# Kernel optimization log

Hardware: AMD Instinct MI355X
Metric: run time of the kernel (lower is better)

The kernel has to match this reference:

```python
import jax, jax.numpy as jnp
import numpy as np

B, P, K, KS = 512, 64, 30, 4      # graphs, nodes per graph, sort-pool k, conv1d kernel
N, E, F, H = B * P, 524288, 128, 256
N_CLASSES = 10
L_OUT = K - KS + 1                 # 27, conv1d output length


def _sage(h, wl, wr, b, src, dst, inv_deg):
    # PyG SAGEConv (mean aggr): out = lin_l(mean_j x_j) + lin_r(x_i); bias only on lin_l
    agg = jax.ops.segment_sum(h[src], dst, num_segments=N) * inv_deg
    return jax.nn.relu(agg @ wl + b + h @ wr)


def setup_inputs() -> dict:
    key = jax.random.key(0)
    ks = jax.random.split(key, 32)
    x = jax.random.normal(ks[0], (N, F), jnp.float32)
    # intra-graph random edges (src -> dst aggregation)
    g = jax.random.randint(ks[1], (E,), 0, B)
    src = g * P + jax.random.randint(ks[2], (E,), 0, P)
    dst = g * P + jax.random.randint(ks[3], (E,), 0, P)
    edge_index = jnp.stack([src, dst]).astype(jnp.int32)
    batch = jnp.repeat(jnp.arange(B), P).astype(jnp.int32)  # sorted graph ids

    def lin(k, i, o):
        return jax.random.normal(k, (i, o), jnp.float32) / np.float32(np.sqrt(i))

    inp = {"x": x, "edge_index": edge_index, "batch": batch}
    dims = [(F, H), (H, H), (H, H), (H, H)]
    ki = 4
    for li, (i, o) in enumerate(dims):
        inp[f"sage{li}_wl"] = lin(ks[ki], i, o); ki += 1
        inp[f"sage{li}_wr"] = lin(ks[ki], i, o); ki += 1
        inp[f"sage{li}_b"] = jnp.zeros((o,), jnp.float32)
    inp["conv1d_w"] = jax.random.normal(ks[ki], (H, H, KS), jnp.float32) / np.float32(np.sqrt(H * KS)); ki += 1
    inp["conv1d_b"] = jnp.zeros((H,), jnp.float32)
    inp["lin1_w"] = lin(ks[ki], H * L_OUT, H); ki += 1
    inp["lin1_b"] = jnp.zeros((H,), jnp.float32)
    inp["lin2_w"] = lin(ks[ki], H, 128); ki += 1
    inp["lin2_b"] = jnp.zeros((128,), jnp.float32)
    inp["out_w"] = lin(ks[ki], 128, N_CLASSES); ki += 1
    inp["out_b"] = jnp.zeros((N_CLASSES,), jnp.float32)
    return inp


def reference(x, edge_index, batch,
              sage0_wl, sage0_wr, sage0_b,
              sage1_wl, sage1_wr, sage1_b,
              sage2_wl, sage2_wr, sage2_b,
              sage3_wl, sage3_wr, sage3_b,
              conv1d_w, conv1d_b, lin1_w, lin1_b,
              lin2_w, lin2_b, out_w, out_b):
    src, dst = edge_index[0], edge_index[1]
    deg = jax.ops.segment_sum(jnp.ones(src.shape, x.dtype), dst, num_segments=N)
    inv_deg = (1.0 / jnp.maximum(deg, 1.0))[:, None]

    h = jnp.nan_to_num(x, nan=0.0)
    h = _sage(h, sage0_wl, sage0_wr, sage0_b, src, dst, inv_deg)
    h = _sage(h, sage1_wl, sage1_wr, sage1_b, src, dst, inv_deg)
    h = _sage(h, sage2_wl, sage2_wr, sage2_b, src, dst, inv_deg)
    h = _sage(h, sage3_wl, sage3_wr, sage3_b, src, dst, inv_deg)  # [N, H]

    # SortAggregation(k=K): to dense batch, sort by last channel desc, top-k, zero-pad
    counts = jax.ops.segment_sum(jnp.ones(N, jnp.int32), batch, num_segments=B)
    offsets = jnp.cumsum(counts) - counts
    pos = jnp.arange(N) - offsets[batch]
    D = h.shape[1]
    dense = jnp.zeros((B, P, D), h.dtype).at[batch, pos].set(h)
    valid = jnp.zeros((B, P), bool).at[batch, pos].set(True)
    skey = jnp.where(valid, dense[..., -1], -jnp.inf)
    order = jnp.argsort(-skey, axis=1)[:, :K]                       # [B, K]
    topk = jnp.take_along_axis(dense, order[..., None], axis=1)     # [B, K, D]
    tvalid = jnp.take_along_axis(valid, order, axis=1)
    topk = jnp.where(tvalid[..., None], topk, 0.0)

    # x.view(B, K, -1).permute(0, 2, 1) -> [B, D, K]
    xc = topk.transpose(0, 2, 1)
    y = jax.lax.conv_general_dilated(xc, conv1d_w, (1,), 'VALID',
                                     dimension_numbers=('NCH', 'OIH', 'NCH'))
    y = jax.nn.relu(y + conv1d_b[None, :, None])                    # [B, H, L_OUT]
    y = y.reshape(B, -1)                                            # dropout is identity in eval
    y = jax.nn.relu(y @ lin1_w + lin1_b)
    y = jax.nn.relu(y @ lin2_w + lin2_b)
    return jax.nn.relu(y @ out_w + out_b)                           # [B, N_CLASSES]
```

## Files before the change

kernel.cpp:

```cpp
#include <hip/hip_runtime.h>
#include <hip/hip_bf16.h>

#define NNODES 32768
#define NEDGES 524288
#define NGRAPH 512
#define PNODES 64
#define KTOP 30
#define FIN 128
#define HID 256
#define LOUT 27

#define C1F 4.8828125e-4f
#define C2F 2.384185791015625e-7f

using f16x8 = __attribute__((ext_vector_type(8))) _Float16;
using f16x4 = __attribute__((ext_vector_type(4))) _Float16;
using f32x4 = __attribute__((ext_vector_type(4))) float;
using f32x16 = __attribute__((ext_vector_type(16))) float;
using u32x4 = __attribute__((ext_vector_type(4))) uint32_t;

template<int N> struct IC { static constexpr int v = N; };

#define GLDS(src, dst) __builtin_amdgcn_global_load_lds( \
    (const __attribute__((address_space(1))) void*)(src), \
    (__attribute__((address_space(3))) void*)(dst), 16, 0, 0)

__global__ void hist_kernel(const int* __restrict__ dst, int* __restrict__ counts) {
    int e = blockIdx.x * blockDim.x + threadIdx.x;
    if (e < NEDGES) atomicAdd(&counts[dst[e]], 1);
}

__global__ __launch_bounds__(1024) void scan_block_kernel(const int* __restrict__ counts,
        int* __restrict__ loc, int* __restrict__ partial) {
    int b = blockIdx.x, t = threadIdx.x;
    int i = b * 1024 + t;
    int v = counts[i];
    int lane = t & 63, w = t >> 6;
    int x = v;
    #pragma unroll
    for (int d = 1; d < 64; d <<= 1) { int y = __shfl_up(x, d, 64); if (lane >= d) x += y; }
    __shared__ int ws[16];
    if (lane == 63) ws[w] = x;
    __syncthreads();
    if (w == 0) {
        int s = (lane < 16) ? ws[lane] : 0;
        #pragma unroll
        for (int d = 1; d < 16; d <<= 1) { int y = __shfl_up(s, d, 64); if (lane >= d) s += y; }
        if (lane < 16) ws[lane] = s;
    }
    __syncthreads();
    int base = (w > 0) ? ws[w - 1] : 0;
    int incl = base + x;
    loc[i] = incl - v;
    if (t == 1023) partial[b] = incl;
}

__global__ __launch_bounds__(1024) void scan_fixup_kernel(const int* __restrict__ loc,
        const int* __restrict__ partial, const int* __restrict__ counts,
        int* __restrict__ offsets, int* __restrict__ cursor, float* __restrict__ invdeg) {
    int b = blockIdx.x, t = threadIdx.x;
    int i = b * 1024 + t;
    __shared__ int sbase;
    if (t == 0) { int s = 0; for (int j = 0; j < b; ++j) s += partial[j]; sbase = s; }
    __syncthreads();
    int o = loc[i] + sbase;
    offsets[i] = o;
    cursor[i] = o;
    invdeg[i] = 1.0f / fmaxf((float)counts[i], 1.0f);
}

__global__ void scatter_kernel(const int* __restrict__ src, const int* __restrict__ dst,
        int* __restrict__ cursor, int* __restrict__ ssrc) {
    int e = blockIdx.x * blockDim.x + threadIdx.x;
    if (e < NEDGES) {
        int d = dst[e];
        int p = atomicAdd(&cursor[d], 1);
        ssrc[p] = ((d & 63) << 6) | (src[e] & 63);
    }
}

struct PrepSage {
    const float* src[8];
    _Float16* dh[8];
    _Float16* dl[8];
    int logK[8];
    int part[8];
};

struct PrepAll {
    const float* x;
    _Float16* h0h; _Float16* h0l;
    PrepSage ps;
    const float* convw; _Float16* cvh; _Float16* cvl;
    const float* l1w; _Float16* w1h; _Float16* w1l;
};

__global__ __launch_bounds__(256) void prep_all_kernel(PrepAll P) {
    __shared__ float sh[64][65];
    const int b = blockIdx.x, t = threadIdx.x;
    if (b < 4096) {
        int i = b * 256 + t;
        float4 v = *(const float4*)(P.x + (size_t)i * 4);
        float xs[4] = {v.x, v.y, v.z, v.w};
        f16x4 hh, ll;
        #pragma unroll
        for (int q = 0; q < 4; ++q) {
            float a = xs[q];
            a = (a != a) ? 0.f : a;
            _Float16 h = (_Float16)a;
            hh[q] = h;
            ll[q] = (_Float16)((a - (float)h) * 2048.0f);
        }
        *(f16x4*)(P.h0h + (size_t)i * 4) = hh;
        *(f16x4*)(P.h0l + (size_t)i * 4) = ll;
    } else if (b < 6144) {
        int seg = b - 4096;
        int y = seg >> 8;
        int idx = (seg & 255) * 256 + t;
        int lk = P.ps.logK[y], K = 1 << lk;
        if (idx < 256 * K) {
            int n = idx >> lk, k = idx & (K - 1);
            float w = P.ps.src[y][(size_t)k * 256 + n];
            _Float16 h = (_Float16)w;
            int wv = n >> 5, l31 = n & 31;
            int c = k >> 5, h2 = (k >> 4) & 1, hb = (k >> 3) & 1, j = k & 7;
            int NCH = K >> 5;
            size_t dst = (size_t)(wv * 2 + P.ps.part[y]) * (size_t)(NCH * 1024)
                       + (size_t)(c * 2 + h2) * 512 + (size_t)(hb * 32 + l31) * 8 + j;
            P.ps.dh[y][dst] = h;
            P.ps.dl[y][dst] = (_Float16)((w - (float)h) * 2048.0f);
        }
    } else if (b < 7168) {
        int idx = (b - 6144) * 256 + t;
        int o = idx >> 10, k = idx & 1023;
        float w = P.convw[(size_t)o * 1024 + (k & 255) * 4 + (k >> 8)];
        _Float16 h = (_Float16)w;
        P.cvh[(size_t)o * 1024 + k] = h;
        P.cvl[(size_t)o * 1024 + k] = (_Float16)((w - (float)h) * 2048.0f);
    } else {
        int seg = b - 7168;
        int kb = (seg % 108) * 64;
        int nb = (seg / 108) * 64;
        {
            int kk = t >> 2;
            int nc = (t & 3) * 16;
            int k = kb + kk, l = k >> 8, c = k & 255;
            const float* srow = P.l1w + (size_t)(c * 27 + l) * 256 + nb + nc;
            #pragma unroll
            for (int j = 0; j < 16; j += 4) {
                float4 v = *(const float4*)(srow + j);
                sh[kk][nc + j + 0] = v.x;
                sh[kk][nc + j + 1] = v.y;
                sh[kk][nc + j + 2] = v.z;
                sh[kk][nc + j + 3] = v.w;
            }
        }
        __syncthreads();
        {
            int nn = t >> 2;
            int kc = (t & 3) * 16;
            f16x8 oh[2], ol[2];
            #pragma unroll
            for (int j = 0; j < 16; ++j) {
                float x = sh[kc + j][nn];
                _Float16 h = (_Float16)x;
                oh[j >> 3][j & 7] = h;
                ol[j >> 3][j & 7] = (_Float16)((x - (float)h) * 2048.0f);
            }
            size_t o = (size_t)(nb + nn) * 6912 + kb + kc;
            *(f16x8*)(P.w1h + o) = oh[0];
            *(f16x8*)(P.w1h + o + 8) = oh[1];
            *(f16x8*)(P.w1l + o) = ol[0];
            *(f16x8*)(P.w1l + o + 8) = ol[1];
        }
    }
}

struct SageWAll {
    const _Float16* wh[4];
    const _Float16* wl[4];
    const float* bias[4];
};

__global__ __launch_bounds__(512, 2) void fused_sage_all_kernel(
        const _Float16* __restrict__ hh, const _Float16* __restrict__ hl,
        const int* __restrict__ offsets, const int* __restrict__ counts,
        const int* __restrict__ ssrc, const float* __restrict__ invdeg,
        SageWAll W,
        _Float16* __restrict__ tkh, _Float16* __restrict__ tkl) {
    __shared__ __align__(16) _Float16 hp[2][8 * 2048];
    __shared__ __align__(16) uint32_t Sw[4096];
    const int g = blockIdx.x, t = threadIdx.x;
    const int lane = t & 63, wave = t >> 6;
    const int l31 = lane & 31, hb = lane >> 5;

    #pragma unroll
    for (int i = 0; i < 8; ++i) Sw[t + i * 512] = 0;

    {
        int a = lane >> 2, b = lane & 3;
        #pragma unroll
        for (int u0 = 0; u0 < 4; ++u0) {
            int u = u0 * 8 + wave;
            int part = u & 1;
            int cs = u >> 1;
            int c = cs >> 2, stripe = cs & 3;
            int row = stripe * 16 + a;
            int o = b ^ ((row >> 1) & 3) ^ (c & 3);
            const _Float16* src = (part ? hl : hh) + (size_t)g * (64 * FIN)
                                + (size_t)row * FIN + c * 32 + o * 8;
            GLDS(src, &hp[part][c * 2048 + stripe * 512]);
        }
    }
    const int gbeg = offsets[g * 64];
    const int gend = offsets[g * 64 + 63] + counts[g * 64 + 63];
    __syncthreads();

    for (int e = gbeg + t; e < gend; e += 512)
        atomicAdd(&Sw[ssrc[e] & 4095], 1u);
    __syncthreads();

    {
        int d = t >> 3, o = t & 7;
        float idg = invdeg[g * 64 + d];
        float v[8];
        #pragma unroll
        for (int j = 0; j < 8; ++j) v[j] = (float)Sw[(d << 6) + (o << 3) + j] * idg;
        __syncthreads();
        _Float16* Sp = (_Float16*)Sw;
        f16x8 s0, s1;
        #pragma unroll
        for (int j = 0; j < 8; ++j) {
            _Float16 h1 = (_Float16)v[j];
            s0[j] = h1;
            s1[j] = (_Float16)((v[j] - (float)h1) * 2048.0f);
        }
        int addr = (d << 6) + ((o ^ (d & 7)) << 3);
        *(f16x8*)&Sp[addr] = s0;
        *(f16x8*)&Sp[4096 + addr] = s1;
    }
    __syncthreads();

    const int col = (wave << 5) + l31;

    auto gemmHalf = [&](auto NC, const _Float16* __restrict__ Bh,
                        const _Float16* __restrict__ Bl, int rowOff) -> f32x16 {
        constexpr int NIT = decltype(NC)::v * 2;
        const int lo8 = lane << 3;
        f32x16 a0 = 0.f, a1 = 0.f;
        f16x8 bhN = *(const f16x8*)(Bh + lo8);
        f16x8 blN = *(const f16x8*)(Bl + lo8);
        #pragma unroll
        for (int it = 0; it < NIT; ++it) {
            const int c = it >> 1, h2 = it & 1;
            f16x8 bh = bhN, bl = blN;
            if (it + 1 < NIT) {
                bhN = *(const f16x8*)(Bh + (it + 1) * 512 + lo8);
                blN = *(const f16x8*)(Bl + (it + 1) * 512 + lo8);
            }
            const int slot = (2 * h2 + hb) ^ ((l31 >> 1) & 3) ^ (c & 3);
            const int addr = rowOff + c * 2048 + (l31 << 5) + (slot << 3);
            f16x8 ah = *(const f16x8*)&hp[0][addr];
            f16x8 al = *(const f16x8*)&hp[1][addr];
            a0 = __builtin_amdgcn_mfma_f32_32x32x16_f16(ah, bh, a0, 0, 0, 0);
            a1 = __builtin_amdgcn_mfma_f32_32x32x16_f16(al, bh, a1, 0, 0, 0);
            a1 = __builtin_amdgcn_mfma_f32_32x32x16_f16(ah, bl, a1, 0, 0, 0);
        }
        return a0 + C1F * a1;
    };

    auto packpair = [](float x, float y, uint32_t& hw, uint32_t& lw) {
        _Float16 xh = (_Float16)x, yh = (_Float16)y;
        _Float16 xl = (_Float16)((x - (float)xh) * 2048.0f);
        _Float16 yl = (_Float16)((y - (float)yh) * 2048.0f);
        hw = (uint32_t)__builtin_bit_cast(unsigned short, xh)
           | ((uint32_t)__builtin_bit_cast(unsigned short, yh) << 16);
        lw = (uint32_t)__builtin_bit_cast(unsigned short, xl)
           | ((uint32_t)__builtin_bit_cast(unsigned short, yl) << 16);
    };

    auto spass = [&](int soffBase, const f32x16& pf0, const f32x16& pf1, f32x16& qf) {
        const _Float16* Sp = (const _Float16*)Sw;
        f32x16 sA = 0.f, sB = 0.f;
        #pragma unroll
        for (int kc = 0; kc < 4; ++kc) {
            const f32x16& pfk = (kc < 2) ? pf0 : pf1;
            const int i0 = ((2 * kc) & 3) * 4, i1 = ((2 * kc + 1) & 3) * 4;
            float kv0 = hb ? pfk[i1 + 0] : pfk[i0 + 0];
            float kv1 = hb ? pfk[i1 + 1] : pfk[i0 + 1];
            float kv2 = hb ? pfk[i1 + 2] : pfk[i0 + 2];
            float kv3 = hb ? pfk[i1 + 3] : pfk[i0 + 3];
            float sv0 = hb ? pfk[i0 + 0] : pfk[i1 + 0];
            float sv1 = hb ? pfk[i0 + 1] : pfk[i1 + 1];
            float sv2 = hb ? pfk[i0 + 2] : pfk[i1 + 2];
            float sv3 = hb ? pfk[i0 + 3] : pfk[i1 + 3];
            uint32_t kh0, kl0, kh1, kl1, sh0, sl0, sh1, sl1;
            packpair(kv0, kv1, kh0, kl0);
            packpair(kv2, kv3, kh1, kl1);
            packpair(sv0, sv1, sh0, sl0);
            packpair(sv2, sv3, sh1, sl1);
            uint32_t rh0 = (uint32_t)__shfl_xor((int)sh0, 32, 64);
            uint32_t rh1 = (uint32_t)__shfl_xor((int)sh1, 32, 64);
            uint32_t rl0 = (uint32_t)__shfl_xor((int)sl0, 32, 64);
            uint32_t rl1 = (uint32_t)__shfl_xor((int)sl1, 32, 64);
            u32x4 bhu, blu;
            bhu[0] = hb ? rh0 : kh0;  bhu[1] = hb ? rh1 : kh1;
            bhu[2] = hb ? kh0 : rh0;  bhu[3] = hb ? kh1 : rh1;
            blu[0] = hb ? rl0 : kl0;  blu[1] = hb ? rl1 : kl1;
            blu[2] = hb ? kl0 : rl0;  blu[3] = hb ? kl1 : rl1;
            f16x8 bhv = __builtin_bit_cast(f16x8, bhu);
            f16x8 blv = __builtin_bit_cast(f16x8, blu);
            int soff = soffBase + (l31 << 6) + (((2 * kc + hb) ^ (l31 & 7)) << 3);
            f16x8 s0a = *(const f16x8*)&Sp[soff];
            f16x8 s1a = *(const f16x8*)&Sp[4096 + soff];
            sA = __builtin_amdgcn_mfma_f32_32x32x16_f16(s0a, bhv, sA, 0, 0, 0);
            sB = __builtin_amdgcn_mfma_f32_32x32x16_f16(s0a, blv, sB, 0, 0, 0);
            sB = __builtin_amdgcn_mfma_f32_32x32x16_f16(s1a, bhv, sB, 0, 0, 0);
        }
        qf += sA + C1F * sB;
    };

    auto run_layer = [&](auto NC, const _Float16* __restrict__ Wsh,
                         const _Float16* __restrict__ Wsl,
                         const float* __restrict__ bias,
                         f32x16& sC0, f32x16& sC1) {
        constexpr size_t wstride = (size_t)decltype(NC)::v * 1024;
        const _Float16* BqH = Wsh + (size_t)((wave << 1) + 1) * wstride;
        const _Float16* BqL = Wsl + (size_t)((wave << 1) + 1) * wstride;
        const _Float16* BpH = Wsh + (size_t)(wave << 1) * wstride;
        const _Float16* BpL = Wsl + (size_t)(wave << 1) * wstride;
        f32x16 qf0 = gemmHalf(NC, BqH, BqL, 0);
        f32x16 qf1 = gemmHalf(NC, BqH, BqL, 1024);
        f32x16 pf0 = gemmHalf(NC, BpH, BpL, 0);
        f32x16 pf1 = gemmHalf(NC, BpH, BpL, 1024);
        spass(0, pf0, pf1, qf0);
        spass(2048, pf0, pf1, qf1);
        const float bb = bias[col];
        #pragma unroll
        for (int reg = 0; reg < 16; ++reg) {
            sC0[reg] = fmaxf(qf0[reg] + bb, 0.f);
            sC1[reg] = fmaxf(qf1[reg] + bb, 0.f);
        }
    };

    auto hp_write = [&](const f32x16& sC0, const f32x16& sC1) {
        int oc = l31 >> 3, j = l31 & 7;
        #pragma unroll
        for (int mi = 0; mi < 2; ++mi)
            #pragma unroll
            for (int reg = 0; reg < 16; ++reg) {
                int row = (mi << 5) + (reg & 3) + ((reg >> 2) << 3) + (hb << 2);
                int slot = oc ^ ((row >> 1) & 3) ^ (wave & 3);
                int addr = wave * 2048 + (row << 5) + (slot << 3) + j;
                float v = mi ? sC1[reg] : sC0[reg];
                _Float16 h1 = (_Float16)v;
                hp[0][addr] = h1;
                hp[1][addr] = (_Float16)((v - (float)h1) * 2048.0f);
            }
    };

    f32x16 sC0, sC1;
    run_layer(IC<4>{}, W.wh[0], W.wl[0], W.bias[0], sC0, sC1);
    __syncthreads();
    hp_write(sC0, sC1);
    __syncthreads();
    run_layer(IC<8>{}, W.wh[1], W.wl[1], W.bias[1], sC0, sC1);
    __syncthreads();
    hp_write(sC0, sC1);
    __syncthreads();
    run_layer(IC<8>{}, W.wh[2], W.wl[2], W.bias[2], sC0, sC1);
    __syncthreads();
    hp_write(sC0, sC1);
    __syncthreads();
    run_layer(IC<8>{}, W.wh[3], W.wl[3], W.bias[3], sC0, sC1);
    __syncthreads();

    #pragma unroll
    for (int mi = 0; mi < 2; ++mi) {
        #pragma unroll
        for (int reg = 0; reg < 16; ++reg) {
            int row = (mi << 5) + (reg & 3) + ((reg >> 2) << 3) + (hb << 2);
            int cx = col ^ ((((row >> 2) & 1) << 5) | ((row & 3) << 3));
            float v = mi ? sC1[reg] : sC0[reg];
            _Float16 h1 = (_Float16)v;
            hp[0][(row << 8) + cx] = h1;
            hp[1][(row << 8) + cx] = (_Float16)((v - (float)h1) * 2048.0f);
        }
    }
    __syncthreads();

    float* vals = (float*)Sw;
    int* ords = (int*)(Sw + 64);
    if (t < 64) {
        int sx = 255 ^ ((((t >> 2) & 1) << 5) | ((t & 3) << 3));
        vals[t] = (float)hp[0][(t << 8) + sx] + C1F * (float)hp[1][(t << 8) + sx];
    }
    __syncthreads();
    if (t < 64) {
        float v = vals[t];
        int rank = 0;
        for (int j = 0; j < 64; ++j) {
            float vj = vals[j];
            rank += (vj > v) || (vj == v && j < t);
        }
        if (rank < KTOP) ords[rank] = t;
    }
    __syncthreads();
    for (int r = wave; r < KTOP; r += 8) {
        int row = ords[r];
        int cc = (lane & 31) << 3;
        int sx = cc ^ ((((row >> 2) & 1) << 5) | ((row & 3) << 3));
        size_t d = (size_t)(g * KTOP + r) * HID + cc;
        if (lane < 32) *(f16x8*)(tkh + d) = *(const f16x8*)&hp[0][(row << 8) + sx];
        else           *(f16x8*)(tkl + d) = *(const f16x8*)&hp[1][(row << 8) + sx];
    }
}

template<int NPROD, int CONV, int NPAIRS, int EPI>
__global__ __launch_bounds__(256, 2) void mfma_ps_kernel(
        const _Float16* __restrict__ A1h, const _Float16* __restrict__ A1l,
        const _Float16* __restrict__ A2h, const _Float16* __restrict__ A2l,
        const _Float16* __restrict__ B1h, const _Float16* __restrict__ B1l,
        const _Float16* __restrict__ B2h, const _Float16* __restrict__ B2l,
        const float* __restrict__ bias,
        _Float16* __restrict__ outh, _Float16* __restrict__ outl,
        float* __restrict__ Cpart,
        int lda, int K, int Nd, int nrb) {
    __shared__ _Float16 As[2][2][128 * 32];
    __shared__ _Float16 Bs[2][2][128 * 32];
    const int t = threadIdx.x;
    const int lane = t & 63, wave = t >> 6;
    const int wr = wave & 1, wc = wave >> 1;
    const int bid = blockIdx.x;
    const int rb = bid % nrb, cb = bid / nrb;
    const int row0 = rb * 128, col0 = cb * 128;
    const int l31 = lane & 31, hb = lane >> 5, x3 = l31 & 3;
    const int r16 = lane >> 2;
    const int qsrc8 = ((lane & 3) ^ (r16 & 3)) * 8;
    size_t aoffj[2], boffj[2];
    #pragma unroll
    for (int j = 0; j < 2; ++j) {
        int ar = row0 + wave * 32 + j * 16 + r16;
        aoffj[j] = CONV ? ((size_t)ar * 256 + (size_t)(ar / 27) * 768)
                        : (size_t)ar * (size_t)lda;
        boffj[j] = (size_t)(col0 + wave * 32 + j * 16 + r16) * (size_t)K;
    }
    int aroff[2], broff[2], slot8[2];
    #pragma unroll
    for (int mi = 0; mi < 2; ++mi) aroff[mi] = (wr * 64 + mi * 32 + l31) * 32;
    #pragma unroll
    for (int ni = 0; ni < 2; ++ni) broff[ni] = (wc * 64 + ni * 32 + l31) * 32;
    #pragma unroll
    for (int h = 0; h < 2; ++h) slot8[h] = ((2 * h + hb) ^ x3) * 8;

    const int KV = NPAIRS * K;
    const int kchunk = KV / gridDim.z;
    const int kv_lo = blockIdx.z * kchunk, kv_hi = kv_lo + kchunk;

    f32x16 acc0[2][2], acc1[2][2], acc2[2][2];
    #pragma unroll
    for (int i = 0; i < 2; ++i)
        #pragma unroll
        for (int j = 0; j < 2; ++j) { acc0[i][j] = 0.f; acc1[i][j] = 0.f; acc2[i][j] = 0.f; }

    auto stage = [&](int kv, int b) {
        int p = (NPAIRS == 2 && kv >= K) ? 1 : 0;
        int k = kv - p * K;
        const _Float16* __restrict__ sAh = p ? A2h : A1h;
        const _Float16* __restrict__ sAl = p ? A2l : A1l;
        const _Float16* __restrict__ sBh = p ? B2h : B1h;
        const _Float16* __restrict__ sBl = p ? B2l : B1l;
        #pragma unroll
        for (int j = 0; j < 2; ++j) {
            int ldsbase = (wave * 32 + j * 16) * 32;
            size_t ga = aoffj[j] + k + qsrc8;
            size_t gb = boffj[j] + k + qsrc8;
            GLDS(sAh + ga, &As[b][0][ldsbase]);
            GLDS(sAl + ga, &As[b][1][ldsbase]);
            GLDS(sBh + gb, &Bs[b][0][ldsbase]);
            GLDS(sBl + gb, &Bs[b][1][ldsbase]);
        }
    };

    stage(kv_lo, 0);
    __syncthreads();
    int b = 0;
    for (int kv = kv_lo; kv < kv_hi; kv += 32) {
        if (kv + 32 < kv_hi) stage(kv + 32, b ^ 1);
        #pragma unroll
        for (int h = 0; h < 2; ++h) {
            f16x8 af0[2], af1[2], bf0[2], bf1[2];
            #pragma unroll
            for (int mi = 0; mi < 2; ++mi) {
                af0[mi] = *(const f16x8*)&As[b][0][aroff[mi] + slot8[h]];
                af1[mi] = *(const f16x8*)&As[b][1][aroff[mi] + slot8[h]];
            }
            #pragma unroll
            for (int ni = 0; ni < 2; ++ni) {
                bf0[ni] = *(const f16x8*)&Bs[b][0][broff[ni] + slot8[h]];
                bf1[ni] = *(const f16x8*)&Bs[b][1][broff[ni] + slot8[h]];
            }
            #pragma unroll
            for (int mi = 0; mi < 2; ++mi)
                #pragma unroll
                for (int ni = 0; ni < 2; ++ni) {
                    acc0[mi][ni] = __builtin_amdgcn_mfma_f32_32x32x16_f16(af0[mi], bf0[ni], acc0[mi][ni], 0, 0, 0);
                    acc1[mi][ni] = __builtin_amdgcn_mfma_f32_32x32x16_f16(af1[mi], bf0[ni], acc1[mi][ni], 0, 0, 0);
                    acc1[mi][ni] = __builtin_amdgcn_mfma_f32_32x32x16_f16(af0[mi], bf1[ni], acc1[mi][ni], 0, 0, 0);
                    if (NPROD == 4)
                        acc2[mi][ni] = __builtin_amdgcn_mfma_f32_32x32x16_f16(af1[mi], bf1[ni], acc2[mi][ni], 0, 0, 0);
                }
        }
        b ^= 1;
        __syncthreads();
    }

    const int rquad = 4 * hb;
    #pragma unroll
    for (int ni = 0; ni < 2; ++ni) {
        int col = col0 + wc * 64 + ni * 32 + l31;
        float bb = (EPI == 0) ? bias[col] : 0.f;
        #pragma unroll
        for (int mi = 0; mi < 2; ++mi) {
            #pragma unroll
            for (int reg = 0; reg < 16; ++reg) {
                float v = acc0[mi][ni][reg] + C1F * acc1[mi][ni][reg];
                if (NPROD == 4) v += C2F * acc2[mi][ni][reg];
                int row = row0 + wr * 64 + mi * 32 + (reg & 3) + 8 * (reg >> 2) + rquad;
                if (EPI == 0) {
                    v = fmaxf(v + bb, 0.f);
                    _Float16 h = (_Float16)v;
                    size_t o = (size_t)row * Nd + col;
                    outh[o] = h;
                    outl[o] = (_Float16)((v - (float)h) * 2048.0f);
                } else {
                    size_t zb = (size_t)blockIdx.z * (size_t)(nrb * 128) * Nd;
                    Cpart[zb + (size_t)row * Nd + col] = v;
                }
            }
        }
    }
}

__global__ void reduce_conv_kernel(const float* __restrict__ yb32,
        const float* __restrict__ b, _Float16* __restrict__ ybh, _Float16* __restrict__ ybl) {
    int i = blockIdx.x * 256 + threadIdx.x;
    float v = fmaxf(yb32[i] + yb32[i + 13824 * 256] + b[i & 255], 0.f);
    _Float16 h = (_Float16)v;
    ybh[i] = h;
    ybl[i] = (_Float16)((v - (float)h) * 2048.0f);
}

__global__ void reduce_lin1_kernel(const float* __restrict__ z1p,
        const float* __restrict__ b, float* __restrict__ z1) {
    int i = blockIdx.x * 256 + threadIdx.x;
    float s = b[i & 255];
    #pragma unroll
    for (int z = 0; z < 27; ++z) s += z1p[(size_t)z * 131072 + i];
    z1[i] = fmaxf(s, 0.f);
}

__global__ __launch_bounds__(256) void gemm64_kernel(
        const float* __restrict__ A, const float* __restrict__ B,
        const float* __restrict__ bias, float* __restrict__ C,
        int lda, int kend, int Nd) {
    __shared__ float As[16][64];
    __shared__ float Bs[16][64];
    const int tid = threadIdx.x;
    const int tx = tid & 15, ty = tid >> 4;
    const int la_r = tid >> 2, la_c = (tid & 3) << 2;
    const int lb_r = tid >> 4, lb_c = (tid & 15) << 2;
    const int row0 = blockIdx.x * 64, col0 = blockIdx.y * 64;
    const size_t aoff = (size_t)(row0 + la_r) * (size_t)lda;
    float acc[4][4] = {};
    for (int k0 = 0; k0 < kend; k0 += 16) {
        __syncthreads();
        float4 av = *(const float4*)(A + aoff + k0 + la_c);
        As[la_c + 0][la_r] = av.x;
        As[la_c + 1][la_r] = av.y;
        As[la_c + 2][la_r] = av.z;
        As[la_c + 3][la_r] = av.w;
        *(float4*)&Bs[lb_r][lb_c] = *(const float4*)(B + (size_t)(k0 + lb_r) * Nd + col0 + lb_c);
        __syncthreads();
        #pragma unroll
        for (int k = 0; k < 16; ++k) {
            float4 a = *(const float4*)&As[k][ty << 2];
            float4 b = *(const float4*)&Bs[k][tx << 2];
            acc[0][0] += a.x * b.x; acc[0][1] += a.x * b.y; acc[0][2] += a.x * b.z; acc[0][3] += a.x * b.w;
            acc[1][0] += a.y * b.x; acc[1][1] += a.y * b.y; acc[1][2] += a.y * b.z; acc[1][3] += a.y * b.w;
            acc[2][0] += a.z * b.x; acc[2][1] += a.z * b.y; acc[2][2] += a.z * b.z; acc[2][3] += a.z * b.w;
            acc[3][0] += a.w * b.x; acc[3][1] += a.w * b.y; acc[3][2] += a.w * b.z; acc[3][3] += a.w * b.w;
        }
    }
    #pragma unroll
    for (int i = 0; i < 4; ++i) {
        int row = row0 + (ty << 2) + i;
        #pragma unroll
        for (int j = 0; j < 4; ++j) {
            int col = col0 + (tx << 2) + j;
            C[(size_t)row * Nd + col] = fmaxf(acc[i][j] + bias[col], 0.f);
        }
    }
}

__global__ void out_kernel(const float* __restrict__ z2, const float* __restrict__ w,
        const float* __restrict__ b, float* __restrict__ out) {
    int idx = blockIdx.x * blockDim.x + threadIdx.x;
    if (idx < NGRAPH * 10) {
        int r = idx / 10, c = idx % 10;
        float s = b[c];
        for (int k = 0; k < 128; ++k) s += z2[r * 128 + k] * w[k * 10 + c];
        out[idx] = fmaxf(s, 0.f);
    }
}

extern "C" void kernel_launch(void* const* d_in, const int* in_sizes, int n_in,
                              void* d_out, int out_size, void* d_ws, size_t ws_size,
                              hipStream_t stream) {
    const float* x    = (const float*)d_in[0];
    const int*   edge = (const int*)d_in[1];
    const int*   esrc = edge;
    const int*   edst = edge + NEDGES;
    const float* wl[4] = {(const float*)d_in[3], (const float*)d_in[6], (const float*)d_in[9],  (const float*)d_in[12]};
    const float* wr[4] = {(const float*)d_in[4], (const float*)d_in[7], (const float*)d_in[10], (const float*)d_in[13]};
    const float* sb[4] = {(const float*)d_in[5], (const float*)d_in[8], (const float*)d_in[11], (const float*)d_in[14]};
    const float* convw = (const float*)d_in[15];
    const float* convb = (const float*)d_in[16];
    const float* l1w   = (const float*)d_in[17];
    const float* l1b   = (const float*)d_in[18];
    const float* l2w   = (const float*)d_in[19];
    const float* l2b   = (const float*)d_in[20];
    const float* ow    = (const float*)d_in[21];
    const float* ob    = (const float*)d_in[22];
    float* out = (float*)d_out;

    char* ws = (char*)d_ws;
    size_t off = 0;
    auto alloc = [&](size_t bytes) -> char* {
        char* p = ws + off;
        off = (off + bytes + 255) & ~(size_t)255;
        return p;
    };
    int*   counts  = (int*)alloc((size_t)NNODES * 4);
    int*   offsets = (int*)alloc((size_t)NNODES * 4);
    int*   cursor  = (int*)alloc((size_t)NNODES * 4);
    int*   loc     = (int*)alloc((size_t)NNODES * 4);
    int*   partial = (int*)alloc(32 * 4);
    float* invdeg  = (float*)alloc((size_t)NNODES * 4);
    int*   ssrc    = (int*)alloc((size_t)NEDGES * 4);
    _Float16* wch[4]; _Float16* wcl[4];
    for (int l = 0; l < 4; ++l) {
        size_t kb = (size_t)512 * (l ? HID : FIN) * 2;
        wch[l] = (_Float16*)alloc(kb);
        wcl[l] = (_Float16*)alloc(kb);
    }
    _Float16* cvh = (_Float16*)alloc((size_t)HID * 1024 * 2);
    _Float16* cvl = (_Float16*)alloc((size_t)HID * 1024 * 2);

    const size_t H0T = (size_t)NNODES * FIN * 2;
    const size_t AGT = (size_t)NNODES * HID * 2;
    const size_t TKT = (size_t)NGRAPH * KTOP * HID * 2;
    const size_t YBT = (size_t)NGRAPH * LOUT * HID * 2;
    const size_t YB32T = (size_t)2 * 13824 * 256 * 4;
    const size_t W1T = (size_t)HID * 6912 * 2;

    char* R1 = alloc(2 * H0T);
    char* R2 = alloc(2 * AGT);
    char* R3 = alloc(2 * AGT);
    char* R4 = alloc(2 * AGT);
    _Float16* h0h = (_Float16*)R1; _Float16* h0l = (_Float16*)(R1 + H0T);
    _Float16* tkh = (_Float16*)R4; _Float16* tkl = (_Float16*)(R4 + TKT);
    _Float16* ybh = (_Float16*)R2; _Float16* ybl_ = (_Float16*)(R2 + YBT);
    float* yb32 = (float*)(R2 + 2 * YBT);
    float* z1p  = (float*)(R2 + 2 * YBT);
    char* tail2 = R2 + 2 * YBT + YB32T;
    float* z1  = (float*)tail2;
    float* z2  = (float*)(tail2 + (size_t)NGRAPH * HID * 4);
    _Float16* w1h = (_Float16*)(tail2 + (size_t)NGRAPH * HID * 4 + (size_t)NGRAPH * 128 * 4 + 256);
    _Float16* w1l = (_Float16*)((char*)w1h + W1T);

    hipMemsetAsync(counts, 0, (size_t)NNODES * 4, stream);
    hist_kernel<<<NEDGES / 256, 256, 0, stream>>>(edst, counts);
    scan_block_kernel<<<NNODES / 1024, 1024, 0, stream>>>(counts, loc, partial);
    scan_fixup_kernel<<<NNODES / 1024, 1024, 0, stream>>>(loc, partial, counts, offsets, cursor, invdeg);
    scatter_kernel<<<NEDGES / 256, 256, 0, stream>>>(esrc, edst, cursor, ssrc);

    PrepAll pa;
    pa.x = x; pa.h0h = h0h; pa.h0l = h0l;
    for (int l = 0; l < 4; ++l) {
        int lk = l ? 8 : 7;
        pa.ps.src[2 * l] = wl[l];     pa.ps.dh[2 * l] = wch[l];     pa.ps.dl[2 * l] = wcl[l];
        pa.ps.src[2 * l + 1] = wr[l]; pa.ps.dh[2 * l + 1] = wch[l]; pa.ps.dl[2 * l + 1] = wcl[l];
        pa.ps.logK[2 * l] = lk;     pa.ps.part[2 * l] = 0;
        pa.ps.logK[2 * l + 1] = lk; pa.ps.part[2 * l + 1] = 1;
    }
    pa.convw = convw; pa.cvh = cvh; pa.cvl = cvl;
    pa.l1w = l1w; pa.w1h = w1h; pa.w1l = w1l;
    prep_all_kernel<<<7600, 256, 0, stream>>>(pa);

    SageWAll swa;
    for (int l = 0; l < 4; ++l) { swa.wh[l] = wch[l]; swa.wl[l] = wcl[l]; swa.bias[l] = sb[l]; }
    fused_sage_all_kernel<<<NGRAPH, 512, 0, stream>>>(
        h0h, h0l, offsets, counts, ssrc, invdeg, swa, tkh, tkl);

    mfma_ps_kernel<3, 1, 1, 1><<<dim3(108 * 2, 1, 2), 256, 0, stream>>>(
        tkh, tkl, nullptr, nullptr, cvh, cvl, nullptr, nullptr, nullptr, nullptr, nullptr, yb32, 256, 1024, HID, 108);
    reduce_conv_kernel<<<13824 * 256 / 256, 256, 0, stream>>>(yb32, convb, ybh, ybl_);

    mfma_ps_kernel<3, 0, 1, 1><<<dim3(4 * 2, 1, 27), 256, 0, stream>>>(
        ybh, ybl_, nullptr, nullptr, w1h, w1l, nullptr, nullptr, nullptr, nullptr, nullptr, z1p, 6912, 6912, HID, 4);
    reduce_lin1_kernel<<<NGRAPH * HID / 256, 256, 0, stream>>>(z1p, l1b, z1);

    gemm64_kernel<<<dim3(NGRAPH / 64, 128 / 64), 256, 0, stream>>>(z1, l2w, l2b, z2, HID, HID, 128);

    out_kernel<<<(NGRAPH * 10 + 255) / 256, 256, 0, stream>>>(z2, ow, ob, out);
}
```

Before: 433.2 us.

## Fuse conv1d split-K reduce into GEMM epilogue and reorder SAGE layer GEMM/pack

The conv1d GEMM no longer splits K across two z-slices. It now uses the EPI==0 epilogue, which adds the bias, applies ReLU and writes the fp16 hi/lo outputs directly, so the separate reduce_conv kernel and its fp32 partial buffer go away. Inside the fused SAGE kernel, the P-half GEMM and its fp16 packing now run before the Q-half GEMM, and the packed operands are kept in registers for both S passes. This is meant to overlap the pack and shuffle work with MFMA and avoid packing twice. The cost is higher register pressure and half as many conv blocks, which means less parallelism in that GEMM.

```diff
diff --git a/kernel.cpp b/kernel.cpp
--- a/kernel.cpp
+++ b/kernel.cpp
@@ -279,9 +279,20 @@
            | ((uint32_t)__builtin_bit_cast(unsigned short, yl) << 16);
     };
 
-    auto spass = [&](int soffBase, const f32x16& pf0, const f32x16& pf1, f32x16& qf) {
-        const _Float16* Sp = (const _Float16*)Sw;
-        f32x16 sA = 0.f, sB = 0.f;
+    auto run_layer = [&](auto NC, const _Float16* __restrict__ Wsh,
+                         const _Float16* __restrict__ Wsl,
+                         const float* __restrict__ bias,
+                         f32x16& sC0, f32x16& sC1) {
+        constexpr size_t wstride = (size_t)decltype(NC)::v * 1024;
+        const _Float16* BpH = Wsh + (size_t)(wave << 1) * wstride;
+        const _Float16* BpL = Wsl + (size_t)(wave << 1) * wstride;
+        const _Float16* BqH = Wsh + (size_t)((wave << 1) + 1) * wstride;
+        const _Float16* BqL = Wsl + (size_t)((wave << 1) + 1) * wstride;
+
+        f32x16 pf0 = gemmHalf(NC, BpH, BpL, 0);
+        f32x16 pf1 = gemmHalf(NC, BpH, BpL, 1024);
+
+        f16x8 bhA[4], blA[4];
         #pragma unroll
         for (int kc = 0; kc < 4; ++kc) {
             const f32x16& pfk = (kc < 2) ? pf0 : pf1;
@@ -308,33 +319,41 @@
             bhu[2] = hb ? kh0 : rh0;  bhu[3] = hb ? kh1 : rh1;
             blu[0] = hb ? rl0 : kl0;  blu[1] = hb ? rl1 : kl1;
             blu[2] = hb ? kl0 : rl0;  blu[3] = hb ? kl1 : rl1;
-            f16x8 bhv = __builtin_bit_cast(f16x8, bhu);
-            f16x8 blv = __builtin_bit_cast(f16x8, blu);
-            int soff = soffBase + (l31 << 6) + (((2 * kc + hb) ^ (l31 & 7)) << 3);
-            f16x8 s0a = *(const f16x8*)&Sp[soff];
-            f16x8 s1a = *(const f16x8*)&Sp[4096 + soff];
-            sA = __builtin_amdgcn_mfma_f32_32x32x16_f16(s0a, bhv, sA, 0, 0, 0);
-            sB = __builtin_amdgcn_mfma_f32_32x32x16_f16(s0a, blv, sB, 0, 0, 0);
-            sB = __builtin_amdgcn_mfma_f32_32x32x16_f16(s1a, bhv, sB, 0, 0, 0);
-        }
-        qf += sA + C1F * sB;
-    };
-
-    auto run_layer = [&](auto NC, const _Float16* __restrict__ Wsh,
-                         const _Float16* __restrict__ Wsl,
-                         const float* __restrict__ bias,
-                         f32x16& sC0, f32x16& sC1) {
-        constexpr size_t wstride = (size_t)decltype(NC)::v * 1024;
-        const _Float16* BqH = Wsh + (size_t)((wave << 1) + 1) * wstride;
-        const _Float16* BqL = Wsl + (size_t)((wave << 1) + 1) * wstride;
-        const _Float16* BpH = Wsh + (size_t)(wave << 1) * wstride;
-        const _Float16* BpL = Wsl + (size_t)(wave << 1) * wstride;
+            bhA[kc] = __builtin_bit_cast(f16x8, bhu);
+            blA[kc] = __builtin_bit_cast(f16x8, blu);
+        }
+
         f32x16 qf0 = gemmHalf(NC, BqH, BqL, 0);
         f32x16 qf1 = gemmHalf(NC, BqH, BqL, 1024);
-        f32x16 pf0 = gemmHalf(NC, BpH, BpL, 0);
-        f32x16 pf1 = gemmHalf(NC, BpH, BpL, 1024);
-        spass(0, pf0, pf1, qf0);
-        spass(2048, pf0, pf1, qf1);
+
+        const _Float16* Sp = (const _Float16*)Sw;
+        {
+            f32x16 sA = 0.f, sB = 0.f;
+            #pragma unroll
+            for (int kc = 0; kc < 4; ++kc) {
+                int soff = (l31 << 6) + (((2 * kc + hb) ^ (l31 & 7)) << 3);
+                f16x8 s0a = *(const f16x8*)&Sp[soff];
+                f16x8 s1a = *(const f16x8*)&Sp[4096 + soff];
+                sA = __builtin_amdgcn_mfma_f32_32x32x16_f16(s0a, bhA[kc], sA, 0, 0, 0);
+                sB = __builtin_amdgcn_mfma_f32_32x32x16_f16(s0a, blA[kc], sB, 0, 0, 0);
+                sB = __builtin_amdgcn_mfma_f32_32x32x16_f16(s1a, bhA[kc], sB, 0, 0, 0);
+            }
+            qf0 += sA + C1F * sB;
+        }
+        {
+            f32x16 sA = 0.f, sB = 0.f;
+            #pragma unroll
+            for (int kc = 0; kc < 4; ++kc) {
+                int soff = 2048 + (l31 << 6) + (((2 * kc + hb) ^ (l31 & 7)) << 3);
+                f16x8 s0a = *(const f16x8*)&Sp[soff];
+                f16x8 s1a = *(const f16x8*)&Sp[4096 + soff];
+                sA = __builtin_amdgcn_mfma_f32_32x32x16_f16(s0a, bhA[kc], sA, 0, 0, 0);
+                sB = __builtin_amdgcn_mfma_f32_32x32x16_f16(s0a, blA[kc], sB, 0, 0, 0);
+                sB = __builtin_amdgcn_mfma_f32_32x32x16_f16(s1a, bhA[kc], sB, 0, 0, 0);
+            }
+            qf1 += sA + C1F * sB;
+        }
+
         const float bb = bias[col];
         #pragma unroll
         for (int reg = 0; reg < 16; ++reg) {
@@ -542,15 +561,6 @@
     }
 }
 
-__global__ void reduce_conv_kernel(const float* __restrict__ yb32,
-        const float* __restrict__ b, _Float16* __restrict__ ybh, _Float16* __restrict__ ybl) {
-    int i = blockIdx.x * 256 + threadIdx.x;
-    float v = fmaxf(yb32[i] + yb32[i + 13824 * 256] + b[i & 255], 0.f);
-    _Float16 h = (_Float16)v;
-    ybh[i] = h;
-    ybl[i] = (_Float16)((v - (float)h) * 2048.0f);
-}
-
 __global__ void reduce_lin1_kernel(const float* __restrict__ z1p,
         const float* __restrict__ b, float* __restrict__ z1) {
     int i = blockIdx.x * 256 + threadIdx.x;
@@ -671,7 +681,6 @@
     _Float16* h0h = (_Float16*)R1; _Float16* h0l = (_Float16*)(R1 + H0T);
     _Float16* tkh = (_Float16*)R4; _Float16* tkl = (_Float16*)(R4 + TKT);
     _Float16* ybh = (_Float16*)R2; _Float16* ybl_ = (_Float16*)(R2 + YBT);
-    float* yb32 = (float*)(R2 + 2 * YBT);
     float* z1p  = (float*)(R2 + 2 * YBT);
     char* tail2 = R2 + 2 * YBT + YB32T;
     float* z1  = (float*)tail2;
@@ -703,9 +712,8 @@
     fused_sage_all_kernel<<<NGRAPH, 512, 0, stream>>>(
         h0h, h0l, offsets, counts, ssrc, invdeg, swa, tkh, tkl);
 
-    mfma_ps_kernel<3, 1, 1, 1><<<dim3(108 * 2, 1, 2), 256, 0, stream>>>(
-        tkh, tkl, nullptr, nullptr, cvh, cvl, nullptr, nullptr, nullptr, nullptr, nullptr, yb32, 256, 1024, HID, 108);
-    reduce_conv_kernel<<<13824 * 256 / 256, 256, 0, stream>>>(yb32, convb, ybh, ybl_);
+    mfma_ps_kernel<3, 1, 1, 0><<<dim3(108 * 2, 1, 1), 256, 0, stream>>>(
+        tkh, tkl, nullptr, nullptr, cvh, cvl, nullptr, nullptr, convb, ybh, ybl_, nullptr, 256, 1024, HID, 108);
 
     mfma_ps_kernel<3, 0, 1, 1><<<dim3(4 * 2, 1, 27), 256, 0, stream>>>(
         ybh, ybl_, nullptr, nullptr, w1h, w1l, nullptr, nullptr, nullptr, nullptr, nullptr, z1p, 6912, 6912, HID, 4);
```

New measurement: 554.5 us. 1.28x slower.
